# Kernel tuning notes

Measured on AMD Instinct MI355X. Metric: run time of the kernel, lower is better.

## Reference

```python
import jax, jax.numpy as jnp
import numpy as np

DIM = 256
HEADS = 4
HEAD_DIM = DIM // HEADS
SCALE = HEAD_DIM ** -0.5


def setup_inputs() -> dict:
    key = jax.random.key(0)
    k_x, k_wqkv, k_bqkv, k_wp, k_bp = jax.random.split(key, 5)
    B, N = 8, 2048
    x = jax.random.normal(k_x, (B, N, DIM), dtype=jnp.float32)
    # torch nn.Linear weights: [out_features, in_features]
    W_qkv = jax.random.normal(k_wqkv, (3 * DIM, DIM), dtype=jnp.float32) * (DIM ** -0.5)
    b_qkv = jax.random.normal(k_bqkv, (3 * DIM,), dtype=jnp.float32) * 0.02
    W_proj = jax.random.normal(k_wp, (DIM, DIM), dtype=jnp.float32) * (DIM ** -0.5)
    b_proj = jax.random.normal(k_bp, (DIM,), dtype=jnp.float32) * 0.02
    return {"x": x, "W_qkv": W_qkv, "b_qkv": b_qkv, "W_proj": W_proj, "b_proj": b_proj}


def reference(x, W_qkv, b_qkv, W_proj, b_proj):
    B, N, C = x.shape
    h, d = HEADS, HEAD_DIM
    # fused QKV projection: [B,N,3C] -> [3,B,h,N,d]
    qkv = (jnp.einsum('bnc,oc->bno', x, W_qkv) + b_qkv)
    qkv = qkv.reshape(B, N, 3, h, d).transpose(2, 0, 3, 1, 4)
    q, k, v = qkv[0], qkv[1], qkv[2]
    # full N x N score matrix, as in the original module
    attn = jnp.einsum('bhnd,bhmd->bhnm', q, k) * SCALE
    attn = jax.nn.softmax(attn, axis=-1)
    out = jnp.einsum('bhnm,bhmd->bhnd', attn, v)  # [B,h,N,d]
    out = out.transpose(0, 2, 1, 3).reshape(B, N, C)
    return jnp.einsum('bnc,oc->bno', out, W_proj) + b_proj
```

## Files before the change

kernel.cpp:

```cpp
#include <hip/hip_runtime.h>
#include <hip/hip_bf16.h>


typedef __bf16 bf16x8 __attribute__((ext_vector_type(8)));
typedef float f32x4 __attribute__((ext_vector_type(4)));
typedef float f32x16 __attribute__((ext_vector_type(16)));
typedef unsigned u32x2 __attribute__((ext_vector_type(2)));

#define MFMA16(a, b, c) __builtin_amdgcn_mfma_f32_16x16x32_bf16((a), (b), (c), 0, 0, 0)
#define MFMA32(a, b, c) __builtin_amdgcn_mfma_f32_32x32x16_bf16((a), (b), (c), 0, 0, 0)

#define C2 0.18033688011112042f

#if __has_builtin(__builtin_amdgcn_exp2f)
__device__ __forceinline__ float fexp2(float x) { return __builtin_amdgcn_exp2f(x); }
#else
__device__ __forceinline__ float fexp2(float x) {
    float r;
    asm("v_exp_f32 %0, %1" : "=v"(r) : "v"(x));
    return r;
}
#endif

__device__ __forceinline__ bf16x8 ldg8(const __bf16* p) {
    return *reinterpret_cast<const bf16x8*>(p);
}

__device__ __forceinline__ bf16x8 cvt8(const float* p) {
    const f32x4 a = *reinterpret_cast<const f32x4*>(p);
    const f32x4 b = *reinterpret_cast<const f32x4*>(p + 4);
    bf16x8 r;
    r[0] = (__bf16)a[0]; r[1] = (__bf16)a[1]; r[2] = (__bf16)a[2]; r[3] = (__bf16)a[3];
    r[4] = (__bf16)b[0]; r[5] = (__bf16)b[1]; r[6] = (__bf16)b[2]; r[7] = (__bf16)b[3];
    return r;
}

__device__ __forceinline__ unsigned pk2(float a, float b) {
    __bf16 x = (__bf16)a, y = (__bf16)b;
    unsigned short ux = __builtin_bit_cast(unsigned short, x);
    unsigned short uy = __builtin_bit_cast(unsigned short, y);
    return (unsigned)ux | ((unsigned)uy << 16);
}

__global__ __launch_bounds__(256) void cvt_all(
    const float* __restrict__ X, const float* __restrict__ Wq,
    const float* __restrict__ Wp, __bf16* __restrict__ Xb,
    __bf16* __restrict__ Wqb, __bf16* __restrict__ Wpb)
{
    const int g = blockIdx.x * 256 + threadIdx.x;
    const float* src;
    __bf16* dst;
    int off;
    if (g < 524288)      { src = X;  dst = Xb;  off = g; }
    else if (g < 548864) { src = Wq; dst = Wqb; off = g - 524288; }
    else                 { src = Wp; dst = Wpb; off = g - 548864; }
    *reinterpret_cast<bf16x8*>(dst + (size_t)off * 8) = cvt8(src + (size_t)off * 8);
}

__global__ __launch_bounds__(256) void qkv_gemm(
    const __bf16* __restrict__ X, const __bf16* __restrict__ Wq,
    const float* __restrict__ bq, __bf16* __restrict__ Qw,
    __bf16* __restrict__ Kw, __bf16* __restrict__ Vt)
{
    const int tid = threadIdx.x;
    const int w = tid >> 6, lane = tid & 63;
    const int lo = lane & 15, hi = lane >> 4;
    const int n0 = blockIdx.x * 128;
    const int m0 = blockIdx.y * 128 + w * 32;

    f32x4 acc[2][8] = {};
    const __bf16* xp = X + (m0 + lo) * 256 + hi * 8;
    const __bf16* wp = Wq + (n0 + lo) * 256 + hi * 8;
    #pragma unroll
    for (int k = 0; k < 256; k += 32) {
        bf16x8 a0 = ldg8(xp + k);
        bf16x8 a1 = ldg8(xp + 16 * 256 + k);
        #pragma unroll
        for (int f = 0; f < 8; ++f) {
            bf16x8 bf = ldg8(wp + f * 16 * 256 + k);
            acc[0][f] = MFMA16(a0, bf, acc[0][f]);
            acc[1][f] = MFMA16(a1, bf, acc[1][f]);
        }
    }

    #pragma unroll
    for (int ni = 0; ni < 8; ++ni) {
        const int col = n0 + ni * 16 + lo;
        const float bias = bq[col];
        const float scale = (col < 256) ? C2 : 1.0f;
        #pragma unroll
        for (int mi = 0; mi < 2; ++mi) {
            #pragma unroll
            for (int r = 0; r < 4; ++r) {
                const int row = m0 + mi * 16 + hi * 4 + r;
                const __bf16 hv = (__bf16)((acc[mi][ni][r] + bias) * scale);
                const int bb = row >> 11, n = row & 2047;
                const int d = col & 63;
                if (col < 256) {
                    const int h = col >> 6;
                    Qw[((bb * 4 + h) * 2048 + n) * 64 + d] = hv;
                } else if (col < 512) {
                    const int h = (col - 256) >> 6;
                    Kw[((bb * 4 + h) * 2048 + n) * 64 + d] = hv;
                } else {
                    const int h = (col - 512) >> 6;
                    Vt[((bb * 4 + h) * 64 + d) * 2048 + n] = hv;
                }
            }
        }
    }
}

__global__ __launch_bounds__(512, 4) void attn_kernel(
    const __bf16* __restrict__ Qw, const __bf16* __restrict__ Kw,
    const __bf16* __restrict__ Vt, __bf16* __restrict__ Ow)
{
    __shared__ __align__(16) char lds[33280];

    const int tid = threadIdx.x;
    const int w = tid >> 6, lane = tid & 63;
    const int l31 = lane & 31, hi5 = lane >> 5;
    const int sw = w & 3;
    const int g  = w >> 2;

    const int bid = blockIdx.x;
    const int work = (bid & 7) * 64 + (bid >> 3);
    const int bh = work >> 4;
    const int qx = work & 15;

    const int q = qx * 128 + sw * 32 + l31;
    const int kvbase = g * 1024;
    const int gbase = g * 16384;

    const __bf16* Qp = Qw + (bh * 2048 + q) * 64 + hi5 * 8;
    bf16x8 Qf[4];
    #pragma unroll
    for (int db = 0; db < 4; ++db) Qf[db] = ldg8(Qp + db * 16);

    const __bf16* Kbase = Kw + (size_t)bh * 2048 * 64;
    const __bf16* Vbase = Vt + (size_t)bh * 64 * 2048;

    const int idx = tid & 255;
    const int krow = idx >> 3, kcol8 = (idx & 7) * 8;
    const int swz = ((idx >> 3) & 7) << 4;
    const int kb0 = gbase + ((idx * 16) ^ swz);
    const int kb1 = gbase + (((idx + 256) * 16) ^ swz);
    const int vb0 = gbase + 8192 + ((idx * 16) ^ swz);
    const int vb1 = gbase + 8192 + (((idx + 256) * 16) ^ swz);

    bf16x8 R0 = ldg8(Kbase + (kvbase + krow) * 64 + kcol8);
    bf16x8 R1 = ldg8(Kbase + (kvbase + krow + 32) * 64 + kcol8);
    bf16x8 R2 = ldg8(Vbase + krow * 2048 + kvbase + kcol8);
    bf16x8 R3 = ldg8(Vbase + (krow + 32) * 2048 + kvbase + kcol8);

    f32x16 oacc0 = (f32x16)0.0f, oacc1 = (f32x16)0.0f;
    float lr = 0.0f;

    for (int t = 0; t < 16; ++t) {
        *reinterpret_cast<bf16x8*>(lds + kb0) = R0;
        *reinterpret_cast<bf16x8*>(lds + kb1) = R1;
        *reinterpret_cast<bf16x8*>(lds + vb0) = R2;
        *reinterpret_cast<bf16x8*>(lds + vb1) = R3;
        __syncthreads();

        if (t < 15) {
            const int kv0n = kvbase + (t + 1) * 64;
            R0 = ldg8(Kbase + (kv0n + krow) * 64 + kcol8);
            R1 = ldg8(Kbase + (kv0n + krow + 32) * 64 + kcol8);
            R2 = ldg8(Vbase + krow * 2048 + kv0n + kcol8);
            R3 = ldg8(Vbase + (krow + 32) * 2048 + kv0n + kcol8);
        }

        f32x16 s0 = (f32x16)0.0f, s1 = (f32x16)0.0f;
        #pragma unroll
        for (int db = 0; db < 4; ++db) {
            const int colb = hi5 * 16 + db * 32;
            bf16x8 k0 = *reinterpret_cast<const bf16x8*>(
                lds + gbase + ((l31 * 128 + colb) ^ ((l31 & 7) << 4)));
            bf16x8 k1 = *reinterpret_cast<const bf16x8*>(
                lds + gbase + (((l31 + 32) * 128 + colb) ^ ((l31 & 7) << 4)));
            s0 = MFMA32(k0, Qf[db], s0);
            s1 = MFMA32(k1, Qf[db], s1);
        }

        float p0[16], p1[16];
        #pragma unroll
        for (int i = 0; i < 16; ++i) p0[i] = fexp2(s0[i]);
        #pragma unroll
        for (int i = 0; i < 16; ++i) p1[i] = fexp2(s1[i]);

        float r0 = 0.f, r1 = 0.f, r2 = 0.f, r3 = 0.f;
        #pragma unroll
        for (int i = 0; i < 4; ++i) {
            r0 += p0[i]; r1 += p0[4 + i]; r2 += p0[8 + i]; r3 += p0[12 + i];
            r0 += p1[i]; r1 += p1[4 + i]; r2 += p1[8 + i]; r3 += p1[12 + i];
        }
        lr += (r0 + r1) + (r2 + r3);

#define PVSTEP(PARR, KH)                                                      \
        {                                                                     \
            _Pragma("unroll")                                                 \
            for (int bb2 = 0; bb2 < 2; ++bb2) {                               \
                const int vcolb = KH * 64 + bb2 * 32 + hi5 * 16;              \
                bf16x8 v0 = *reinterpret_cast<const bf16x8*>(                 \
                    lds + gbase + 8192 + ((l31 * 128 + vcolb) ^ ((l31 & 7) << 4))); \
                bf16x8 v1 = *reinterpret_cast<const bf16x8*>(                 \
                    lds + gbase + 8192 + (((l31 + 32) * 128 + vcolb) ^ ((l31 & 7) << 4))); \
                unsigned w0 = pk2(PARR[8 * bb2 + 0], PARR[8 * bb2 + 1]);      \
                unsigned w1 = pk2(PARR[8 * bb2 + 2], PARR[8 * bb2 + 3]);      \
                unsigned w2 = pk2(PARR[8 * bb2 + 4], PARR[8 * bb2 + 5]);      \
                unsigned w3 = pk2(PARR[8 * bb2 + 6], PARR[8 * bb2 + 7]);      \
                asm volatile("v_permlane32_swap_b32 %0, %1" : "+v"(w0), "+v"(w2)); \
                asm volatile("v_permlane32_swap_b32 %0, %1" : "+v"(w1), "+v"(w3)); \
                union { unsigned u[4]; bf16x8 v; } pb;                        \
                pb.u[0] = w0; pb.u[1] = w1; pb.u[2] = w2; pb.u[3] = w3;       \
                oacc0 = MFMA32(v0, pb.v, oacc0);                              \
                oacc1 = MFMA32(v1, pb.v, oacc1);                              \
            }                                                                 \
        }
        PVSTEP(p0, 0)
        PVSTEP(p1, 1)
#undef PVSTEP
        __syncthreads();
    }

    lr += __shfl_xor(lr, 32);

    float* mb = reinterpret_cast<float*>(lds);
    float* lb = reinterpret_cast<float*>(lds + 32768);
    if (g == 1) {
        #pragma unroll
        for (int i = 0; i < 16; ++i) {
            const int r = (i & 3) + 8 * (i >> 2) + 4 * hi5;
            mb[(sw * 64 + r) * 32 + l31] = oacc0[i];
            mb[(sw * 64 + 32 + r) * 32 + l31] = oacc1[i];
        }
        if (hi5 == 0) lb[sw * 32 + l31] = lr;
    }
    __syncthreads();
    if (g == 0) {
        #pragma unroll
        for (int i = 0; i < 16; ++i) {
            const int r = (i & 3) + 8 * (i >> 2) + 4 * hi5;
            oacc0[i] += mb[(sw * 64 + r) * 32 + l31];
            oacc1[i] += mb[(sw * 64 + 32 + r) * 32 + l31];
        }
        lr += lb[sw * 32 + l31];

        const float invl = 1.0f / lr;
        const int bb = bh >> 2, h = bh & 3;
        __bf16* Op = Ow + ((size_t)(bb * 2048 + q)) * 256 + h * 64 + hi5 * 4;
#define EPI(OACC, DBLK)                                                       \
        {                                                                     \
            _Pragma("unroll")                                                 \
            for (int rq = 0; rq < 4; ++rq) {                                  \
                u32x2 st;                                                     \
                st.x = pk2(OACC[rq * 4 + 0] * invl, OACC[rq * 4 + 1] * invl); \
                st.y = pk2(OACC[rq * 4 + 2] * invl, OACC[rq * 4 + 3] * invl); \
                *reinterpret_cast<u32x2*>(Op + DBLK * 32 + rq * 8) = st;      \
            }                                                                 \
        }
        EPI(oacc0, 0)
        EPI(oacc1, 1)
#undef EPI
    }
}

__global__ __launch_bounds__(256) void proj_gemm(
    const __bf16* __restrict__ A, const __bf16* __restrict__ Wp,
    const float* __restrict__ bp, float* __restrict__ out)
{
    const int tid = threadIdx.x;
    const int w = tid >> 6, lane = tid & 63;
    const int lo = lane & 15, hi = lane >> 4;
    const int n0 = blockIdx.x * 128;
    const int m0 = blockIdx.y * 128 + w * 32;

    f32x4 acc[2][8] = {};
    const __bf16* ap = A + (m0 + lo) * 256 + hi * 8;
    const __bf16* wp = Wp + (n0 + lo) * 256 + hi * 8;
    #pragma unroll
    for (int k = 0; k < 256; k += 32) {
        bf16x8 a0 = ldg8(ap + k);
        bf16x8 a1 = ldg8(ap + 16 * 256 + k);
        #pragma unroll
        for (int f = 0; f < 8; ++f) {
            bf16x8 bf = ldg8(wp + f * 16 * 256 + k);
            acc[0][f] = MFMA16(a0, bf, acc[0][f]);
            acc[1][f] = MFMA16(a1, bf, acc[1][f]);
        }
    }
    #pragma unroll
    for (int ni = 0; ni < 8; ++ni) {
        const int col = n0 + ni * 16 + lo;
        const float bias = bp[col];
        #pragma unroll
        for (int mi = 0; mi < 2; ++mi) {
            #pragma unroll
            for (int r = 0; r < 4; ++r) {
                const int row = m0 + mi * 16 + hi * 4 + r;
                out[row * 256 + col] = acc[mi][ni][r] + bias;
            }
        }
    }
}

extern "C" void kernel_launch(void* const* d_in, const int* in_sizes, int n_in,
                              void* d_out, int out_size, void* d_ws, size_t ws_size,
                              hipStream_t stream)
{
    const float* x  = (const float*)d_in[0];
    const float* Wq = (const float*)d_in[1];
    const float* bq = (const float*)d_in[2];
    const float* Wp = (const float*)d_in[3];
    const float* bp = (const float*)d_in[4];

    __bf16* ws = (__bf16*)d_ws;
    const size_t SZ = (size_t)32 * 2048 * 64;
    __bf16* Xb  = ws;
    __bf16* Wqb = Xb + SZ;
    __bf16* Wpb = Wqb + 196608;
    __bf16* Qw  = Wpb + 65536;
    __bf16* Kw  = Qw + SZ;
    __bf16* Vt  = Kw + SZ;
    __bf16* Ow  = Xb;

    cvt_all<<<2176, 256, 0, stream>>>(x, Wq, Wp, Xb, Wqb, Wpb);
    qkv_gemm<<<dim3(6, 128), 256, 0, stream>>>(Xb, Wqb, bq, Qw, Kw, Vt);
    attn_kernel<<<512, 512, 0, stream>>>(Qw, Kw, Vt, Ow);
    proj_gemm<<<dim3(2, 128), 256, 0, stream>>>(Ow, Wpb, bp, (float*)d_out);
}
```

Measured before the change: 128.4 us.

## Halve attention block size to 4 waves with 64 queries and add MFMA priority hints

The attention kernel now runs 1024 blocks of 256 threads. Each block covers 64 queries instead of 128, still split into two KV halves. Each thread loads four K and four V chunks per tile, since fewer threads share the same LDS tile. s_setprio is raised around the QK and PV MFMA sections so matrix work gets issue priority over other waves. The intent is better occupancy and load balance, at the cost of twice the K/V global traffic per query and more per-thread load registers.

```diff
diff --git a/kernel.cpp b/kernel.cpp
--- a/kernel.cpp
+++ b/kernel.cpp
@@ -111,7 +111,7 @@
     }
 }
 
-__global__ __launch_bounds__(512, 4) void attn_kernel(
+__global__ __launch_bounds__(256, 4) void attn_kernel(
     const __bf16* __restrict__ Qw, const __bf16* __restrict__ Kw,
     const __bf16* __restrict__ Vt, __bf16* __restrict__ Ow)
 {
@@ -120,15 +120,15 @@
     const int tid = threadIdx.x;
     const int w = tid >> 6, lane = tid & 63;
     const int l31 = lane & 31, hi5 = lane >> 5;
-    const int sw = w & 3;
-    const int g  = w >> 2;
+    const int sw = w & 1;
+    const int g  = w >> 1;
 
     const int bid = blockIdx.x;
-    const int work = (bid & 7) * 64 + (bid >> 3);
-    const int bh = work >> 4;
-    const int qx = work & 15;
-
-    const int q = qx * 128 + sw * 32 + l31;
+    const int work = (bid & 7) * 128 + (bid >> 3);
+    const int bh = work >> 5;
+    const int qx = work & 31;
+
+    const int q = qx * 64 + sw * 32 + l31;
     const int kvbase = g * 1024;
     const int gbase = g * 16384;
 
@@ -140,38 +140,47 @@
     const __bf16* Kbase = Kw + (size_t)bh * 2048 * 64;
     const __bf16* Vbase = Vt + (size_t)bh * 64 * 2048;
 
-    const int idx = tid & 255;
-    const int krow = idx >> 3, kcol8 = (idx & 7) * 8;
-    const int swz = ((idx >> 3) & 7) << 4;
-    const int kb0 = gbase + ((idx * 16) ^ swz);
-    const int kb1 = gbase + (((idx + 256) * 16) ^ swz);
-    const int vb0 = gbase + 8192 + ((idx * 16) ^ swz);
-    const int vb1 = gbase + 8192 + (((idx + 256) * 16) ^ swz);
-
-    bf16x8 R0 = ldg8(Kbase + (kvbase + krow) * 64 + kcol8);
-    bf16x8 R1 = ldg8(Kbase + (kvbase + krow + 32) * 64 + kcol8);
-    bf16x8 R2 = ldg8(Vbase + krow * 2048 + kvbase + kcol8);
-    bf16x8 R3 = ldg8(Vbase + (krow + 32) * 2048 + kvbase + kcol8);
+    const int idx = tid & 127;
+    const int rb = idx >> 3;
+    const int col8 = (idx & 7) * 8;
+    int kb[4], vb[4];
+    #pragma unroll
+    for (int c = 0; c < 4; ++c) {
+        const int chunk = idx + c * 128;
+        const int byte = (chunk * 16) ^ (((chunk >> 3) & 7) << 4);
+        kb[c] = gbase + byte;
+        vb[c] = gbase + 8192 + byte;
+    }
+
+    bf16x8 RK[4], RV[4];
+    #pragma unroll
+    for (int c = 0; c < 4; ++c) {
+        RK[c] = ldg8(Kbase + (kvbase + rb + c * 16) * 64 + col8);
+        RV[c] = ldg8(Vbase + (rb + c * 16) * 2048 + kvbase + col8);
+    }
 
     f32x16 oacc0 = (f32x16)0.0f, oacc1 = (f32x16)0.0f;
     float lr = 0.0f;
 
     for (int t = 0; t < 16; ++t) {
-        *reinterpret_cast<bf16x8*>(lds + kb0) = R0;
-        *reinterpret_cast<bf16x8*>(lds + kb1) = R1;
-        *reinterpret_cast<bf16x8*>(lds + vb0) = R2;
-        *reinterpret_cast<bf16x8*>(lds + vb1) = R3;
+        #pragma unroll
+        for (int c = 0; c < 4; ++c) {
+            *reinterpret_cast<bf16x8*>(lds + kb[c]) = RK[c];
+            *reinterpret_cast<bf16x8*>(lds + vb[c]) = RV[c];
+        }
         __syncthreads();
 
         if (t < 15) {
             const int kv0n = kvbase + (t + 1) * 64;
-            R0 = ldg8(Kbase + (kv0n + krow) * 64 + kcol8);
-            R1 = ldg8(Kbase + (kv0n + krow + 32) * 64 + kcol8);
-            R2 = ldg8(Vbase + krow * 2048 + kv0n + kcol8);
-            R3 = ldg8(Vbase + (krow + 32) * 2048 + kv0n + kcol8);
+            #pragma unroll
+            for (int c = 0; c < 4; ++c) {
+                RK[c] = ldg8(Kbase + (kv0n + rb + c * 16) * 64 + col8);
+                RV[c] = ldg8(Vbase + (rb + c * 16) * 2048 + kv0n + col8);
+            }
         }
 
         f32x16 s0 = (f32x16)0.0f, s1 = (f32x16)0.0f;
+        __builtin_amdgcn_s_setprio(1);
         #pragma unroll
         for (int db = 0; db < 4; ++db) {
             const int colb = hi5 * 16 + db * 32;
@@ -182,6 +191,7 @@
             s0 = MFMA32(k0, Qf[db], s0);
             s1 = MFMA32(k1, Qf[db], s1);
         }
+        __builtin_amdgcn_s_setprio(0);
 
         float p0[16], p1[16];
         #pragma unroll
@@ -197,6 +207,7 @@
         }
         lr += (r0 + r1) + (r2 + r3);
 
+        __builtin_amdgcn_s_setprio(1);
 #define PVSTEP(PARR, KH)                                                      \
         {                                                                     \
             _Pragma("unroll")                                                 \
@@ -221,6 +232,7 @@
         PVSTEP(p0, 0)
         PVSTEP(p1, 1)
 #undef PVSTEP
+        __builtin_amdgcn_s_setprio(0);
         __syncthreads();
     }
 
@@ -327,6 +339,6 @@
 
     cvt_all<<<2176, 256, 0, stream>>>(x, Wq, Wp, Xb, Wqb, Wpb);
     qkv_gemm<<<dim3(6, 128), 256, 0, stream>>>(Xb, Wqb, bq, Qw, Kw, Vt);
-    attn_kernel<<<512, 512, 0, stream>>>(Qw, Kw, Vt, Ow);
+    attn_kernel<<<1024, 256, 0, stream>>>(Qw, Kw, Vt, Ow);
     proj_gemm<<<dim3(2, 128), 256, 0, stream>>>(Ow, Wpb, bp, (float*)d_out);
 }
```

Measured after the change: 174.4 us. 1.36x slower.
